# Kernel optimization log

Measured on AMD Instinct MI355X. Metric: run time of the kernel, lower is better.

## Reference

```python
import jax, jax.numpy as jnp
import numpy as np

E = 1024
H = 16
D = E // H  # head_dim = 64
FF = 4 * E
EPS = 1e-5


def layernorm(x, g, b):
    mu = jnp.mean(x, axis=-1, keepdims=True)
    var = jnp.var(x, axis=-1, keepdims=True)
    return (x - mu) * jax.lax.rsqrt(var + EPS) * g + b


def setup_inputs() -> dict:
    key = jax.random.key(0)
    ks = jax.random.split(key, 12)
    s = 1.0 / np.sqrt(E)
    sf = 1.0 / np.sqrt(FF)
    return {
        "x": jax.random.normal(ks[0], (2, 2048, E), dtype=jnp.float32),
        "wq": jax.random.uniform(ks[1], (E, E), jnp.float32, -s, s),
        "wk": jax.random.uniform(ks[2], (E, E), jnp.float32, -s, s),
        "wv": jax.random.uniform(ks[3], (E, E), jnp.float32, -s, s),
        "wo": jax.random.uniform(ks[4], (E, E), jnp.float32, -s, s),
        "bo": jax.random.uniform(ks[5], (E,), jnp.float32, -s, s),
        "g1": jnp.ones((E,), jnp.float32),
        "b1": jnp.zeros((E,), jnp.float32),
        "w1": jax.random.uniform(ks[6], (FF, E), jnp.float32, -s, s),
        "bf1": jax.random.uniform(ks[7], (FF,), jnp.float32, -s, s),
        "w2": jax.random.uniform(ks[8], (E, FF), jnp.float32, -sf, sf),
        "bf2": jax.random.uniform(ks[9], (E,), jnp.float32, -sf, sf),
        "g2": jnp.ones((E,), jnp.float32),
        "b2": jnp.zeros((E,), jnp.float32),
    }


def reference(x, wq, wk, wv, wo, bo, g1, b1, w1, bf1, w2, bf2, g2, b2):
    B, L, _ = x.shape
    # projections (torch Linear: x @ W.T)
    q = (x @ wq.T).reshape(B, L, H, D).transpose(0, 2, 1, 3)  # (B,H,L,D)
    k = (x @ wk.T).reshape(B, L, H, D).transpose(0, 2, 1, 3)
    v = (x @ wv.T).reshape(B, L, H, D).transpose(0, 2, 1, 3)
    scores = jnp.einsum('bhqd,bhkd->bhqk', q, k) / np.sqrt(D)
    attn = jax.nn.softmax(scores, axis=-1)
    ctx = jnp.einsum('bhqk,bhkd->bhqd', attn, v)
    ctx = ctx.transpose(0, 2, 1, 3).reshape(B, L, E)
    attn_out = ctx @ wo.T + bo
    h = layernorm(x + attn_out, g1, b1)
    ff = jax.nn.gelu(h @ w1.T + bf1, approximate=False) @ w2.T + bf2
    return layernorm(h + ff, g2, b2)
```

## Files before the change

kernel.cpp:

```cpp
#include <hip/hip_runtime.h>
#include <hip/hip_bf16.h>
#include <stdint.h>

typedef __bf16 bf16x8 __attribute__((ext_vector_type(8)));
typedef float  f32x4  __attribute__((ext_vector_type(4)));
typedef unsigned short u16;
typedef u16 u16x8 __attribute__((ext_vector_type(8)));

__device__ __forceinline__ u16 f2b(float f) {
  uint32_t u = __builtin_bit_cast(uint32_t, f);
  u += 0x7fffu + ((u >> 16) & 1u);
  return (u16)(u >> 16);
}

__device__ __forceinline__ f32x4 mfma16(bf16x8 a, bf16x8 b, f32x4 c) {
  return __builtin_amdgcn_mfma_f32_16x16x32_bf16(a, b, c, 0, 0, 0);
}

__device__ __forceinline__ void gload_lds16(const void* g, void* l) {
  __builtin_amdgcn_global_load_lds(
      (const __attribute__((address_space(1))) void*)g,
      (__attribute__((address_space(3))) void*)l, 16, 0, 0);
}

__global__ void f2b_all(const float* __restrict__ x,  const float* __restrict__ wq,
                        const float* __restrict__ wk, const float* __restrict__ wv,
                        const float* __restrict__ wo, const float* __restrict__ w1,
                        const float* __restrict__ w2,
                        u16* __restrict__ xb, u16* __restrict__ wqkvb,
                        u16* __restrict__ wob, u16* __restrict__ w1b,
                        u16* __restrict__ w2b) {
  const int i = blockIdx.x * blockDim.x + threadIdx.x;
  const float* src; u16* dst; int off;
  if (i < 524288)        { src = x;  dst = xb;              off = i; }
  else if (i < 655360)   { src = wq; dst = wqkvb;           off = i - 524288; }
  else if (i < 786432)   { src = wk; dst = wqkvb + 1048576; off = i - 655360; }
  else if (i < 917504)   { src = wv; dst = wqkvb + 2097152; off = i - 786432; }
  else if (i < 1048576)  { src = wo; dst = wob;             off = i - 917504; }
  else if (i < 1572864)  { src = w1; dst = w1b;             off = i - 1048576; }
  else                   { src = w2; dst = w2b;             off = i - 1572864; }
  const float4* p = (const float4*)src + (size_t)off * 2;
  float4 a = p[0], b = p[1];
  u16x8 r;
  r[0] = f2b(a.x); r[1] = f2b(a.y); r[2] = f2b(a.z); r[3] = f2b(a.w);
  r[4] = f2b(b.x); r[5] = f2b(b.y); r[6] = f2b(b.z); r[7] = f2b(b.w);
  *((u16x8*)dst + off) = r;
}

template<int MODE>
__global__ __launch_bounds__(256, 3) void gemm_bt(
    const u16* __restrict__ A, const u16* __restrict__ W,
    const float* __restrict__ bias,
    void* __restrict__ o0, void* __restrict__ o1, void* __restrict__ o2,
    int Nsz, int Kstride, int Klen, int ntiles)
{
  __shared__ u16 As[2][128 * 32];
  __shared__ u16 Bs[2][128 * 32];
  const int nbn = Nsz >> 7;
  int bid = blockIdx.x;
  bid = (bid & 7) * ((int)gridDim.x >> 3) + (bid >> 3);
  const int tile = (MODE == 1) ? (bid % ntiles) : bid;
  const int sid  = (MODE == 1) ? (bid / ntiles) : 0;
  const int koff = sid * Klen;
  const int bm = tile / nbn;
  const int bn = tile % nbn;
  const int tid = threadIdx.x;
  const int w = tid >> 6, l = tid & 63;
  const int lh = l >> 4, ll = l & 15;
  const int wr = w >> 1, wc = w & 1;

  f32x4 acc[4][4] = {};

  const u16* Ag = A + (size_t)(bm * 128) * Kstride + koff;
  const u16* Wg = W + (size_t)(bn * 128) * Kstride + koff;

  const int flat0 = (w * 2) * 64 + l;
  const int flat1 = (w * 2 + 1) * 64 + l;

  {
    gload_lds16(Ag + (size_t)(flat0 >> 2) * Kstride + (flat0 & 3) * 8, As[0] + flat0 * 8);
    gload_lds16(Wg + (size_t)(flat0 >> 2) * Kstride + (flat0 & 3) * 8, Bs[0] + flat0 * 8);
    gload_lds16(Ag + (size_t)(flat1 >> 2) * Kstride + (flat1 & 3) * 8, As[0] + flat1 * 8);
    gload_lds16(Wg + (size_t)(flat1 >> 2) * Kstride + (flat1 & 3) * 8, Bs[0] + flat1 * 8);
  }
  __syncthreads();

  const int NS = Klen >> 5;
  int buf = 0;
  for (int s = 0; s < NS; ++s) {
    if (s + 1 < NS) {
      const int k0 = (s + 1) * 32;
      gload_lds16(Ag + (size_t)(flat0 >> 2) * Kstride + k0 + (flat0 & 3) * 8, As[buf ^ 1] + flat0 * 8);
      gload_lds16(Wg + (size_t)(flat0 >> 2) * Kstride + k0 + (flat0 & 3) * 8, Bs[buf ^ 1] + flat0 * 8);
      gload_lds16(Ag + (size_t)(flat1 >> 2) * Kstride + k0 + (flat1 & 3) * 8, As[buf ^ 1] + flat1 * 8);
      gload_lds16(Wg + (size_t)(flat1 >> 2) * Kstride + k0 + (flat1 & 3) * 8, Bs[buf ^ 1] + flat1 * 8);
    }
    bf16x8 af[4], bfr[4];
#pragma unroll
    for (int mi = 0; mi < 4; ++mi)
      af[mi] = *(const bf16x8*)(As[buf] + (wr * 64 + mi * 16 + ll) * 32 + lh * 8);
#pragma unroll
    for (int ni = 0; ni < 4; ++ni)
      bfr[ni] = *(const bf16x8*)(Bs[buf] + (wc * 64 + ni * 16 + ll) * 32 + lh * 8);
    __builtin_amdgcn_s_setprio(1);
#pragma unroll
    for (int mi = 0; mi < 4; ++mi)
#pragma unroll
      for (int ni = 0; ni < 4; ++ni)
        acc[mi][ni] = mfma16(af[mi], bfr[ni], acc[mi][ni]);
    __builtin_amdgcn_s_setprio(0);
    __syncthreads();
    buf ^= 1;
  }

#pragma unroll
  for (int mi = 0; mi < 4; ++mi) {
#pragma unroll
    for (int ni = 0; ni < 4; ++ni) {
      const int col = bn * 128 + wc * 64 + ni * 16 + ll;
#pragma unroll
      for (int i = 0; i < 4; ++i) {
        const int row = bm * 128 + wr * 64 + mi * 16 + lh * 4 + i;
        float v = acc[mi][ni][i];
        if (MODE == 1) {
          float* dst = sid ? (float*)o1 : (float*)o0;
          dst[(size_t)row * Nsz + col] = v;
        } else if (MODE == 2) {
          float xx = v + bias[col];
          float u = xx * (0.7978845608f + 0.0356774081f * xx * xx);
          float t = __builtin_amdgcn_exp2f(u * 2.8853900818f);
          float r = __builtin_amdgcn_rcpf(1.0f + t);
          ((u16*)o0)[(size_t)row * Nsz + col] = f2b(xx * t * r);
        } else {
          const int which = col >> 10;
          const int e = col & 1023;
          const int hh = e >> 6, dd = e & 63;
          const int bb = row >> 11, nl = row & 2047;
          if (which == 0) {
            ((u16*)o0)[((size_t)(bb * 16 + hh) * 2048 + nl) * 64 + dd] = f2b(v * 0.18033688f);
          } else if (which == 1) {
            ((u16*)o1)[((size_t)(bb * 16 + hh) * 2048 + nl) * 64 + dd] = f2b(v);
          } else {
            ((u16*)o2)[((size_t)(bb * 16 + hh) * 64 + dd) * 2048 + nl] = f2b(v);
          }
        }
      }
    }
  }
}

__global__ __launch_bounds__(256, 3) void attn_fwd(
    const u16* __restrict__ Q, const u16* __restrict__ K,
    const u16* __restrict__ Vt, u16* __restrict__ ctx)
{
  __shared__ u16 Ks[2][64 * 64];
  __shared__ u16 Vs[2][64 * 64];
  __shared__ u16 Ps[4][32 * 64];

  const int bh = blockIdx.x & 31;
  const int qt = blockIdx.x >> 5;
  const int tid = threadIdx.x;
  const int w = tid >> 6, l = tid & 63;
  const int lh = l >> 4, ll = l & 15;
  const int q0 = qt * 128 + w * 32;

  bf16x8 qf[2][2];
#pragma unroll
  for (int qh = 0; qh < 2; ++qh) {
    const u16* Qg = Q + ((size_t)bh * 2048 + q0 + qh * 16 + ll) * 64;
#pragma unroll
    for (int kk = 0; kk < 2; ++kk)
      qf[qh][kk] = *(const bf16x8*)(Qg + kk * 32 + lh * 8);
  }

  bf16x8 ones;
  {
    const u16 o = 0x3F80;
#pragma unroll
    for (int i = 0; i < 8; ++i) ones[i] = __builtin_bit_cast(__bf16, o);
  }

  f32x4 cacc[2][4] = {};
  f32x4 lacc[2] = {};
  u16* ps = Ps[w];

  const int f0 = tid, f1 = 256 + tid;
  const int r0 = f0 >> 3, s0 = f0 & 7, g0 = (s0 ^ (r0 & 7)) * 8;
  const int r1 = f1 >> 3, s1 = f1 & 7, g1 = (s1 ^ (r1 & 7)) * 8;

  {
    gload_lds16(K + ((size_t)bh * 2048 + r0) * 64 + g0, Ks[0] + f0 * 8);
    gload_lds16(Vt + ((size_t)bh * 64 + r0) * 2048 + g0, Vs[0] + f0 * 8);
    gload_lds16(K + ((size_t)bh * 2048 + r1) * 64 + g1, Ks[0] + f1 * 8);
    gload_lds16(Vt + ((size_t)bh * 64 + r1) * 2048 + g1, Vs[0] + f1 * 8);
  }
  __syncthreads();

  for (int kt = 0; kt < 32; ++kt) {
    const int b = kt & 1;
    if (kt < 31) {
      const int kn = (kt + 1) * 64;
      gload_lds16(K + ((size_t)bh * 2048 + kn + r0) * 64 + g0, Ks[b ^ 1] + f0 * 8);
      gload_lds16(Vt + ((size_t)bh * 64 + r0) * 2048 + kn + g0, Vs[b ^ 1] + f0 * 8);
      gload_lds16(K + ((size_t)bh * 2048 + kn + r1) * 64 + g1, Ks[b ^ 1] + f1 * 8);
      gload_lds16(Vt + ((size_t)bh * 64 + r1) * 2048 + kn + g1, Vs[b ^ 1] + f1 * 8);
    }

    f32x4 st[2][4];
    __builtin_amdgcn_s_setprio(1);
#pragma unroll
    for (int jb = 0; jb < 4; ++jb) {
      f32x4 a0 = {}, a1 = {};
#pragma unroll
      for (int kk = 0; kk < 2; ++kk) {
        const int r = jb * 16 + ll;
        bf16x8 kf = *(const bf16x8*)(Ks[b] + r * 64 + (((kk * 4 + lh) ^ (r & 7)) * 8));
        a0 = mfma16(kf, qf[0][kk], a0);
        a1 = mfma16(kf, qf[1][kk], a1);
      }
      st[0][jb] = a0; st[1][jb] = a1;
    }
    __builtin_amdgcn_s_setprio(0);

#pragma unroll
    for (int qh = 0; qh < 2; ++qh)
#pragma unroll
      for (int jb = 0; jb < 4; ++jb) {
        const float p0 = __builtin_amdgcn_exp2f(st[qh][jb][0]);
        const float p1 = __builtin_amdgcn_exp2f(st[qh][jb][1]);
        const float p2 = __builtin_amdgcn_exp2f(st[qh][jb][2]);
        const float p3 = __builtin_amdgcn_exp2f(st[qh][jb][3]);
        uint2 pk;
        asm("v_cvt_pk_bf16_f32 %0, %1, %2" : "=v"(pk.x) : "v"(p0), "v"(p1));
        asm("v_cvt_pk_bf16_f32 %0, %1, %2" : "=v"(pk.y) : "v"(p2), "v"(p3));
        *(uint2*)(ps + (qh * 16 + ll) * 64 +
                  (((jb * 2 + (lh >> 1)) ^ (ll & 7)) * 8) + (lh & 1) * 4) = pk;
      }

    asm volatile("s_waitcnt lgkmcnt(0)" ::: "memory");
    __builtin_amdgcn_sched_barrier(0);

    __builtin_amdgcn_s_setprio(1);
#pragma unroll
    for (int kk = 0; kk < 2; ++kk) {
      bf16x8 pf0 = *(const bf16x8*)(ps + ll * 64 + (((kk * 4 + lh) ^ (ll & 7)) * 8));
      bf16x8 pf1 = *(const bf16x8*)(ps + (16 + ll) * 64 + (((kk * 4 + lh) ^ (ll & 7)) * 8));
      lacc[0] = mfma16(pf0, ones, lacc[0]);
      lacc[1] = mfma16(pf1, ones, lacc[1]);
#pragma unroll
      for (int db = 0; db < 4; ++db) {
        const int vr = db * 16 + ll;
        bf16x8 vf = *(const bf16x8*)(Vs[b] + vr * 64 + (((kk * 4 + lh) ^ (vr & 7)) * 8));
        cacc[0][db] = mfma16(pf0, vf, cacc[0][db]);
        cacc[1][db] = mfma16(pf1, vf, cacc[1][db]);
      }
    }
    __builtin_amdgcn_s_setprio(0);
    __syncthreads();
  }

  const int bb = bh >> 4, hh = bh & 15;
#pragma unroll
  for (int qh = 0; qh < 2; ++qh)
#pragma unroll
    for (int db = 0; db < 4; ++db)
#pragma unroll
      for (int i = 0; i < 4; ++i) {
        const float v = cacc[qh][db][i] / lacc[qh][i];
        const size_t orow = (size_t)bb * 2048 + q0 + qh * 16 + lh * 4 + i;
        const size_t ocol = (size_t)hh * 64 + db * 16 + ll;
        ctx[orow * 1024 + ocol] = f2b(v);
      }
}

__global__ __launch_bounds__(256) void ln_fused(
    const float* __restrict__ a,  const float* __restrict__ b0,
    const float* __restrict__ b1, const float* __restrict__ b2,
    const float* __restrict__ b3, const float* __restrict__ bias,
    const float* __restrict__ g,  const float* __restrict__ be,
    float* __restrict__ ho, u16* __restrict__ hb)
{
  const int row = blockIdx.x;
  const int t = threadIdx.x;
  const size_t base = (size_t)row * 1024 + t * 4;
  float4 xa = *(const float4*)(a + base);
  float4 xb = *(const float4*)(b0 + base);
  float v0 = xa.x + xb.x, v1 = xa.y + xb.y, v2 = xa.z + xb.z, v3 = xa.w + xb.w;
  if (b1) {
    float4 xc = *(const float4*)(b1 + base);
    v0 += xc.x; v1 += xc.y; v2 += xc.z; v3 += xc.w;
  }
  if (b2) {
    float4 xc = *(const float4*)(b2 + base);
    v0 += xc.x; v1 += xc.y; v2 += xc.z; v3 += xc.w;
  }
  if (b3) {
    float4 xc = *(const float4*)(b3 + base);
    v0 += xc.x; v1 += xc.y; v2 += xc.z; v3 += xc.w;
  }
  if (bias) {
    float4 xd = *(const float4*)(bias + t * 4);
    v0 += xd.x; v1 += xd.y; v2 += xd.z; v3 += xd.w;
  }
  float s = v0 + v1 + v2 + v3;
  float ss = v0 * v0 + v1 * v1 + v2 * v2 + v3 * v3;
#pragma unroll
  for (int d = 1; d < 64; d <<= 1) {
    s += __shfl_xor(s, d);
    ss += __shfl_xor(ss, d);
  }
  __shared__ float red[8];
  const int w = t >> 6, lid = t & 63;
  if (lid == 0) { red[w] = s; red[4 + w] = ss; }
  __syncthreads();
  s = red[0] + red[1] + red[2] + red[3];
  ss = red[4] + red[5] + red[6] + red[7];
  const float mean = s * (1.0f / 1024.0f);
  const float var = ss * (1.0f / 1024.0f) - mean * mean;
  const float rstd = rsqrtf(var + 1e-5f);
  const float vv[4] = {v0, v1, v2, v3};
#pragma unroll
  for (int i = 0; i < 4; ++i) {
    const int col = t * 4 + i;
    const float hv = (vv[i] - mean) * rstd * g[col] + be[col];
    if (ho) ho[base + i] = hv;
    if (hb) hb[base + i] = f2b(hv);
  }
}

extern "C" void kernel_launch(void* const* d_in, const int* in_sizes, int n_in,
                              void* d_out, int out_size, void* d_ws, size_t ws_size,
                              hipStream_t stream) {
  const float* x   = (const float*)d_in[0];
  const float* wq  = (const float*)d_in[1];
  const float* wk  = (const float*)d_in[2];
  const float* wv  = (const float*)d_in[3];
  const float* wo  = (const float*)d_in[4];
  const float* bo  = (const float*)d_in[5];
  const float* g1  = (const float*)d_in[6];
  const float* b1  = (const float*)d_in[7];
  const float* w1  = (const float*)d_in[8];
  const float* bf1 = (const float*)d_in[9];
  const float* w2  = (const float*)d_in[10];
  const float* bf2 = (const float*)d_in[11];
  const float* g2  = (const float*)d_in[12];
  const float* b2  = (const float*)d_in[13];

  char* ws = (char*)d_ws;
  const size_t MB = 1u << 20;
  u16* xb    = (u16*)(ws + 0);
  u16* wqkv  = (u16*)(ws + 8 * MB);
  u16* wob   = (u16*)(ws + 14 * MB);
  u16* w1b   = (u16*)(ws + 16 * MB);
  u16* w2b   = (u16*)(ws + 24 * MB);
  u16* qb    = (u16*)(ws + 32 * MB);
  u16* kb    = (u16*)(ws + 40 * MB);
  u16* vtb   = (u16*)(ws + 48 * MB);
  u16* ctxb  = (u16*)(ws + 56 * MB);
  float* pA   = (float*)(ws + 64 * MB);
  float* hbuf = (float*)(ws + 80 * MB);
  u16* hbb   = (u16*)(ws + 96 * MB);
  float* wo_p1 = (float*)(ws + 32 * MB);
  u16* ff1   = (u16*)(ws + 32 * MB);
  float* f2_p1 = (float*)(ws + 0);

  f2b_all<<<8192, 256, 0, stream>>>(x, wq, wk, wv, wo, w1, w2, xb, wqkv, wob, w1b, w2b);

  gemm_bt<0><<<768, 256, 0, stream>>>(xb, wqkv, nullptr, qb, kb, vtb, 3072, 1024, 1024, 768);
  attn_fwd<<<512, 256, 0, stream>>>(qb, kb, vtb, ctxb);
  gemm_bt<1><<<512, 256, 0, stream>>>(ctxb, wob, nullptr, pA, wo_p1, nullptr, 1024, 1024, 512, 256);
  ln_fused<<<4096, 256, 0, stream>>>(x, pA, wo_p1, nullptr, nullptr, bo, g1, b1, hbuf, hbb);
  gemm_bt<2><<<1024, 256, 0, stream>>>(hbb, w1b, bf1, ff1, nullptr, nullptr, 4096, 1024, 1024, 1024);
  gemm_bt<1><<<512, 256, 0, stream>>>(ff1, w2b, nullptr, pA, f2_p1, nullptr, 1024, 4096, 2048, 256);
  ln_fused<<<4096, 256, 0, stream>>>(hbuf, pA, f2_p1, nullptr, nullptr, bf2, g2, b2,
                                     (float*)d_out, nullptr);
}
```

Measured before the change: 248.1 us.

## Use 4-way split-K with bf16 partials for Wo and FFN2 GEMMs

The split-K GEMMs for the output projection and the second FFN layer now split K four ways instead of two, launching 1024 blocks instead of 512 to fill more CUs. Their partial sums are stored as bf16 rather than fp32, so the partial traffic is the same as before. The layernorm kernel sums the four bf16 partials, and launch bounds are raised to 4 blocks per SIMD. This trades some precision in the partial sums and adds register pressure for more parallelism.

Measured after the change: 246.1 us. Within noise of the previous version (-0.8%).

```diff
diff --git a/kernel.cpp b/kernel.cpp
--- a/kernel.cpp
+++ b/kernel.cpp
@@ -11,6 +11,11 @@
   uint32_t u = __builtin_bit_cast(uint32_t, f);
   u += 0x7fffu + ((u >> 16) & 1u);
   return (u16)(u >> 16);
+}
+
+__device__ __forceinline__ float b2f(u16 b) {
+  uint32_t u = (uint32_t)b << 16;
+  return __builtin_bit_cast(float, u);
 }
 
 __device__ __forceinline__ f32x4 mfma16(bf16x8 a, bf16x8 b, f32x4 c) {
@@ -48,10 +53,11 @@
 }
 
 template<int MODE>
-__global__ __launch_bounds__(256, 3) void gemm_bt(
+__global__ __launch_bounds__(256, 4) void gemm_bt(
     const u16* __restrict__ A, const u16* __restrict__ W,
     const float* __restrict__ bias,
-    void* __restrict__ o0, void* __restrict__ o1, void* __restrict__ o2,
+    void* __restrict__ o0, void* __restrict__ o1,
+    void* __restrict__ o2, void* __restrict__ o3,
     int Nsz, int Kstride, int Klen, int ntiles)
 {
   __shared__ u16 As[2][128 * 32];
@@ -123,8 +129,9 @@
         const int row = bm * 128 + wr * 64 + mi * 16 + lh * 4 + i;
         float v = acc[mi][ni][i];
         if (MODE == 1) {
-          float* dst = sid ? (float*)o1 : (float*)o0;
-          dst[(size_t)row * Nsz + col] = v;
+          u16* dst = (sid == 0) ? (u16*)o0 : (sid == 1) ? (u16*)o1
+                   : (sid == 2) ? (u16*)o2 : (u16*)o3;
+          dst[(size_t)row * Nsz + col] = f2b(v);
         } else if (MODE == 2) {
           float xx = v + bias[col];
           float u = xx * (0.7978845608f + 0.0356774081f * xx * xx);
@@ -274,9 +281,9 @@
 }
 
 __global__ __launch_bounds__(256) void ln_fused(
-    const float* __restrict__ a,  const float* __restrict__ b0,
-    const float* __restrict__ b1, const float* __restrict__ b2,
-    const float* __restrict__ b3, const float* __restrict__ bias,
+    const float* __restrict__ a,  const u16* __restrict__ p0,
+    const u16* __restrict__ p1,   const u16* __restrict__ p2,
+    const u16* __restrict__ p3,   const float* __restrict__ bias,
     const float* __restrict__ g,  const float* __restrict__ be,
     float* __restrict__ ho, u16* __restrict__ hb)
 {
@@ -284,19 +291,22 @@
   const int t = threadIdx.x;
   const size_t base = (size_t)row * 1024 + t * 4;
   float4 xa = *(const float4*)(a + base);
-  float4 xb = *(const float4*)(b0 + base);
-  float v0 = xa.x + xb.x, v1 = xa.y + xb.y, v2 = xa.z + xb.z, v3 = xa.w + xb.w;
-  if (b1) {
-    float4 xc = *(const float4*)(b1 + base);
-    v0 += xc.x; v1 += xc.y; v2 += xc.z; v3 += xc.w;
-  }
-  if (b2) {
-    float4 xc = *(const float4*)(b2 + base);
-    v0 += xc.x; v1 += xc.y; v2 += xc.z; v3 += xc.w;
-  }
-  if (b3) {
-    float4 xc = *(const float4*)(b3 + base);
-    v0 += xc.x; v1 += xc.y; v2 += xc.z; v3 += xc.w;
+  float v0 = xa.x, v1 = xa.y, v2 = xa.z, v3 = xa.w;
+  {
+    ushort4 c = *(const ushort4*)(p0 + base);
+    v0 += b2f(c.x); v1 += b2f(c.y); v2 += b2f(c.z); v3 += b2f(c.w);
+  }
+  if (p1) {
+    ushort4 c = *(const ushort4*)(p1 + base);
+    v0 += b2f(c.x); v1 += b2f(c.y); v2 += b2f(c.z); v3 += b2f(c.w);
+  }
+  if (p2) {
+    ushort4 c = *(const ushort4*)(p2 + base);
+    v0 += b2f(c.x); v1 += b2f(c.y); v2 += b2f(c.z); v3 += b2f(c.w);
+  }
+  if (p3) {
+    ushort4 c = *(const ushort4*)(p3 + base);
+    v0 += b2f(c.x); v1 += b2f(c.y); v2 += b2f(c.z); v3 += b2f(c.w);
   }
   if (bias) {
     float4 xd = *(const float4*)(bias + t * 4);
@@ -357,21 +367,26 @@
   u16* kb    = (u16*)(ws + 40 * MB);
   u16* vtb   = (u16*)(ws + 48 * MB);
   u16* ctxb  = (u16*)(ws + 56 * MB);
-  float* pA   = (float*)(ws + 64 * MB);
+  u16* sp0   = (u16*)(ws + 64 * MB);
+  u16* sp1   = (u16*)(ws + 72 * MB);
+  u16* sp2   = (u16*)(ws + 0);
+  u16* sp3   = (u16*)(ws + 8 * MB);
   float* hbuf = (float*)(ws + 80 * MB);
   u16* hbb   = (u16*)(ws + 96 * MB);
-  float* wo_p1 = (float*)(ws + 32 * MB);
   u16* ff1   = (u16*)(ws + 32 * MB);
-  float* f2_p1 = (float*)(ws + 0);
 
   f2b_all<<<8192, 256, 0, stream>>>(x, wq, wk, wv, wo, w1, w2, xb, wqkv, wob, w1b, w2b);
 
-  gemm_bt<0><<<768, 256, 0, stream>>>(xb, wqkv, nullptr, qb, kb, vtb, 3072, 1024, 1024, 768);
+  gemm_bt<0><<<768, 256, 0, stream>>>(xb, wqkv, nullptr, qb, kb, vtb, nullptr,
+                                      3072, 1024, 1024, 768);
   attn_fwd<<<512, 256, 0, stream>>>(qb, kb, vtb, ctxb);
-  gemm_bt<1><<<512, 256, 0, stream>>>(ctxb, wob, nullptr, pA, wo_p1, nullptr, 1024, 1024, 512, 256);
-  ln_fused<<<4096, 256, 0, stream>>>(x, pA, wo_p1, nullptr, nullptr, bo, g1, b1, hbuf, hbb);
-  gemm_bt<2><<<1024, 256, 0, stream>>>(hbb, w1b, bf1, ff1, nullptr, nullptr, 4096, 1024, 1024, 1024);
-  gemm_bt<1><<<512, 256, 0, stream>>>(ff1, w2b, nullptr, pA, f2_p1, nullptr, 1024, 4096, 2048, 256);
-  ln_fused<<<4096, 256, 0, stream>>>(hbuf, pA, f2_p1, nullptr, nullptr, bf2, g2, b2,
+  gemm_bt<1><<<1024, 256, 0, stream>>>(ctxb, wob, nullptr, sp0, sp1, sp2, sp3,
+                                       1024, 1024, 256, 256);
+  ln_fused<<<4096, 256, 0, stream>>>(x, sp0, sp1, sp2, sp3, bo, g1, b1, hbuf, hbb);
+  gemm_bt<2><<<1024, 256, 0, stream>>>(hbb, w1b, bf1, ff1, nullptr, nullptr, nullptr,
+                                       4096, 1024, 1024, 1024);
+  gemm_bt<1><<<1024, 256, 0, stream>>>(ff1, w2b, nullptr, sp0, sp1, sp2, sp3,
+                                       1024, 4096, 1024, 256);
+  ln_fused<<<4096, 256, 0, stream>>>(hbuf, sp0, sp1, sp2, sp3, bf2, g2, b2,
                                      (float*)d_out, nullptr);
 }
```
